# Kernel optimization log

Hardware: AMD Instinct MI355X
Metric: run time of the kernel (lower is better)

The kernel has to match this reference:

```python
import jax, jax.numpy as jnp
import numpy as np

D_MODEL = 1024
N_HEADS = 16
CHUNK = 64
EPS = 1e-6


def elu_plus_1(x):
    return jax.nn.elu(x) + 1.0


def setup_inputs() -> dict:
    key = jax.random.key(0)
    kx, kq, kk, kv, ko = jax.random.split(key, 5)
    B, T = 4, 4096
    # xavier_uniform for square (D, D) weights: limit = sqrt(6/(D+D))
    lim = float(np.sqrt(6.0 / (D_MODEL + D_MODEL)))
    mk = lambda k: jax.random.uniform(k, (D_MODEL, D_MODEL), jnp.float32, -lim, lim)
    return {
        "x": jax.random.normal(kx, (B, T, D_MODEL), jnp.float32),
        "W_q": mk(kq),
        "W_k": mk(kk),
        "W_v": mk(kv),
        "W_o": mk(ko),
    }


def reference(x, W_q, W_k, W_v, W_o):
    B, T, D = x.shape
    H = N_HEADS
    dk = D // H
    dv = dk
    C = CHUNK
    N = T // C  # T chosen divisible by chunk size (no padding needed)

    q = (x @ W_q.T).reshape(B, T, H, dk)
    k = (x @ W_k.T).reshape(B, T, H, dk)
    v = (x @ W_v.T).reshape(B, T, H, dv)

    phi_q = elu_plus_1(q).reshape(B, N, C, H, dk)
    phi_k = elu_plus_1(k).reshape(B, N, C, H, dk)
    vc = v.reshape(B, N, C, H, dv)

    # Per-chunk key-value outer products and key sums, then exclusive prefix
    # sums over chunks give the carried state S and normalizer z at each
    # chunk's start (same math as the sequential chunk loop).
    KV = jnp.einsum('bnchk,bnchv->bnhkv', phi_k, vc)      # (B,N,H,dk,dv)
    Ksum = phi_k.sum(axis=2)                               # (B,N,C->sum,H,dk) -> (B,N,H,dk)
    KV_cum = jnp.cumsum(KV, axis=1)
    Ksum_cum = jnp.cumsum(Ksum, axis=1)
    S_prefix = jnp.concatenate([jnp.zeros_like(KV_cum[:, :1]), KV_cum[:, :-1]], axis=1)
    z_prefix = jnp.concatenate([jnp.zeros_like(Ksum_cum[:, :1]), Ksum_cum[:, :-1]], axis=1)

    # Inter-chunk contribution from carried state
    inter = jnp.einsum('bnchk,bnhkv->bnchv', phi_q, S_prefix)   # (B,N,C,H,dv)
    z_inter = jnp.einsum('bnchk,bnhk->bnch', phi_q, z_prefix)   # (B,N,C,H)

    # Intra-chunk causal attention
    mask = jnp.tril(jnp.ones((C, C), dtype=x.dtype))
    attn = jnp.einsum('bnihk,bnjhk->bnhij', phi_q, phi_k) * mask  # (B,N,H,C,C)
    intra = jnp.einsum('bnhij,bnjhv->bnihv', attn, vc)            # (B,N,C,H,dv)
    z_intra = attn.sum(axis=-1).transpose(0, 1, 3, 2)             # (B,N,C,H)

    denom = jnp.clip((z_inter + z_intra)[..., None], 1e-6, None)
    y = (inter + intra) / denom                                   # (B,N,C,H,dv)
    y = y.reshape(B, T, H * dv)
    return y @ W_o.T
```

## Files before the change

### kernel.cpp

```cpp
#include <hip/hip_runtime.h>


typedef unsigned short u16;
typedef float  f32x4 __attribute__((ext_vector_type(4)));
typedef short  b16x8 __attribute__((ext_vector_type(8)));
typedef u16    u16x4 __attribute__((ext_vector_type(4)));
typedef u16    u16x8 __attribute__((ext_vector_type(8)));

#define DEVINL __device__ __forceinline__

DEVINL u16 f2b(float f) {
  unsigned u = __float_as_uint(f);
  return (u16)((u + 0x7fffu + ((u >> 16) & 1u)) >> 16);
}
DEVINL float b2f(u16 s) { return __uint_as_float(((unsigned)s) << 16); }

DEVINL f32x4 mfma16(b16x8 a, b16x8 b, f32x4 c) {
  return __builtin_amdgcn_mfma_f32_16x16x32_bf16(a, b, c, 0, 0, 0);
}

DEVINL float phi_elu1(float v) { return v > 0.f ? v + 1.f : __expf(v); }

__global__ void cvt_kernel(const float* __restrict__ in, u16* __restrict__ out, int n8) {
  int stride = gridDim.x * blockDim.x;
  for (int i = blockIdx.x * blockDim.x + threadIdx.x; i < n8; i += stride) {
    const float* p = in + (size_t)i * 8;
    f32x4 a = *(const f32x4*)p;
    f32x4 b = *(const f32x4*)(p + 4);
    u16x8 o;
    o[0] = f2b(a[0]); o[1] = f2b(a[1]); o[2] = f2b(a[2]); o[3] = f2b(a[3]);
    o[4] = f2b(b[0]); o[5] = f2b(b[1]); o[6] = f2b(b[2]); o[7] = f2b(b[3]);
    *(u16x8*)(out + (size_t)i * 8) = o;
  }
}

template <bool PHI, typename OT>
__global__ __launch_bounds__(512, 2) void gemm256(const u16* __restrict__ A,
                                                  const u16* __restrict__ B,
                                                  OT* __restrict__ C, int M, int N) {
  __shared__ char lds[131072];
  const int tid = threadIdx.x, wid = tid >> 6, l = tid & 63;
  const int l15 = l & 15, lg = l >> 4;
  const int wr = wid >> 2, wc = wid & 3;
  const int ntn = N >> 8;
  const int nwg = gridDim.x, bid = blockIdx.x;
  const int cpx = nwg >> 3;
  const int sb = (bid & 7) * cpx + (bid >> 3);
  const int tm = sb / ntn, tn = sb - tm * ntn;

  const int colX0 = (lg * 16) ^ ((l15 & 7) << 4);
  const int colX1 = (64 + lg * 16) ^ ((l15 & 7) << 4);
  char* ldsA = lds + wr * 16384 + l15 * 128;
  char* ldsB = lds + 32768 + (wc >> 1) * 16384 + ((wc & 1) * 64 + l15) * 128;

  const int srow = tid >> 3;
  const int scol = ((((tid & 7) * 16) ^ ((srow & 7) << 4)) >> 1);
  const u16* sA = A + (size_t)(tm * 256 + srow) * 1024 + scol;
  const u16* sB = B + (size_t)(tn * 256 + srow) * 1024 + scol;
  char* ldsStage = lds + wid * 1024;

#define STAGE(tt, h)                                                            \
  do {                                                                          \
    const u16* s_ = ((h) < 2 ? sA : sB) + (size_t)(((h) & 1) * 128) * 1024 +    \
                    (size_t)(tt) * 64;                                          \
    char* d_ = ldsStage + (((tt) & 1) << 16) + ((h) < 2 ? 0 : 32768) +          \
               (((h) & 1) << 14);                                               \
    __builtin_amdgcn_global_load_lds(                                           \
        (const __attribute__((address_space(1))) void*)(s_),                    \
        (__attribute__((address_space(3))) void*)(d_), 16, 0, 0);               \
    __builtin_amdgcn_global_load_lds(                                           \
        (const __attribute__((address_space(1))) void*)(s_ + 64 * 1024),        \
        (__attribute__((address_space(3))) void*)(d_ + 8192), 16, 0, 0);        \
  } while (0)

  f32x4 acc[8][4];
#pragma unroll
  for (int i = 0; i < 8; i++)
#pragma unroll
    for (int j = 0; j < 4; j++) acc[i][j] = f32x4{0.f, 0.f, 0.f, 0.f};

  STAGE(0, 0); STAGE(0, 1); STAGE(0, 2); STAGE(0, 3);
  STAGE(1, 2); STAGE(1, 3);
  asm volatile("s_waitcnt vmcnt(4)" ::: "memory");
  __builtin_amdgcn_s_barrier();

  b16x8 a0[4], a1[4], b0[4], b1[4];
  for (int t = 0; t < 16; ++t) {
    const int cb = (t & 1) << 16;
#pragma unroll
    for (int fm = 0; fm < 4; fm++) a0[fm] = *(const b16x8*)(ldsA + cb + fm * 2048 + colX0);
#pragma unroll
    for (int fn = 0; fn < 4; fn++) b0[fn] = *(const b16x8*)(ldsB + cb + fn * 2048 + colX0);
    if (t < 15) STAGE(t + 1, 0);
    __builtin_amdgcn_s_barrier();
    asm volatile("s_waitcnt lgkmcnt(0)" ::: "memory");
    __builtin_amdgcn_sched_barrier(0);
    __builtin_amdgcn_s_setprio(1);
#pragma unroll
    for (int fm = 0; fm < 4; fm++)
#pragma unroll
      for (int fn = 0; fn < 4; fn++) acc[fm][fn] = mfma16(a0[fm], b0[fn], acc[fm][fn]);
    __builtin_amdgcn_s_setprio(0);
    __builtin_amdgcn_s_barrier();
#pragma unroll
    for (int fm = 0; fm < 4; fm++) a1[fm] = *(const b16x8*)(ldsA + cb + (4 + fm) * 2048 + colX0);
#pragma unroll
    for (int fn = 0; fn < 4; fn++) b1[fn] = *(const b16x8*)(ldsB + cb + fn * 2048 + colX1);
    if (t < 15) STAGE(t + 1, 1);
    __builtin_amdgcn_s_barrier();
    asm volatile("s_waitcnt lgkmcnt(0)" ::: "memory");
    __builtin_amdgcn_sched_barrier(0);
    __builtin_amdgcn_s_setprio(1);
#pragma unroll
    for (int fm = 0; fm < 4; fm++)
#pragma unroll
      for (int fn = 0; fn < 4; fn++) acc[4 + fm][fn] = mfma16(a1[fm], b0[fn], acc[4 + fm][fn]);
    __builtin_amdgcn_s_setprio(0);
    __builtin_amdgcn_s_barrier();
#pragma unroll
    for (int fm = 0; fm < 4; fm++) a0[fm] = *(const b16x8*)(ldsA + cb + fm * 2048 + colX1);
    if (t < 14) STAGE(t + 2, 2);
    __builtin_amdgcn_s_barrier();
    asm volatile("s_waitcnt lgkmcnt(0)" ::: "memory");
    __builtin_amdgcn_sched_barrier(0);
    __builtin_amdgcn_s_setprio(1);
#pragma unroll
    for (int fm = 0; fm < 4; fm++)
#pragma unroll
      for (int fn = 0; fn < 4; fn++) acc[fm][fn] = mfma16(a0[fm], b1[fn], acc[fm][fn]);
    __builtin_amdgcn_s_setprio(0);
    __builtin_amdgcn_s_barrier();
#pragma unroll
    for (int fm = 0; fm < 4; fm++) a1[fm] = *(const b16x8*)(ldsA + cb + (4 + fm) * 2048 + colX1);
    if (t < 14) STAGE(t + 2, 3);
    __builtin_amdgcn_s_barrier();
    asm volatile("s_waitcnt lgkmcnt(0)" ::: "memory");
    __builtin_amdgcn_sched_barrier(0);
    __builtin_amdgcn_s_setprio(1);
#pragma unroll
    for (int fm = 0; fm < 4; fm++)
#pragma unroll
      for (int fn = 0; fn < 4; fn++) acc[4 + fm][fn] = mfma16(a1[fm], b1[fn], acc[4 + fm][fn]);
    __builtin_amdgcn_s_setprio(0);
    if (t < 14) asm volatile("s_waitcnt vmcnt(4)" ::: "memory");
    else        asm volatile("s_waitcnt vmcnt(0)" ::: "memory");
    __builtin_amdgcn_s_barrier();
  }
#undef STAGE

#pragma unroll
  for (int fm = 0; fm < 8; ++fm)
#pragma unroll
    for (int fn = 0; fn < 4; ++fn)
#pragma unroll
      for (int r = 0; r < 4; ++r) {
        size_t grow = (size_t)tm * 256 + wr * 128 + fm * 16 + lg * 4 + r;
        size_t gcol = (size_t)tn * 256 + wc * 64 + fn * 16 + l15;
        float v = acc[fm][fn][r];
        if (PHI) v = phi_elu1(v);
        OT* p = C + grow * (size_t)N + gcol;
        if constexpr (sizeof(OT) == 2) *p = (OT)f2b(v);
        else                           *p = (OT)v;
      }
}

__global__ __launch_bounds__(256) void transpose64(const u16* __restrict__ in,
                                                   u16* __restrict__ out) {
  __shared__ u16 tile[64][68];
  const int t = threadIdx.x;
  const int tr = blockIdx.x, tc = blockIdx.y;
#pragma unroll
  for (int i = 0; i < 4; i++) {
    int idx = i * 256 + t, r = idx >> 4, c4 = idx & 15;
    u16x4 v = *(const u16x4*)(in + (size_t)(tr * 64 + r) * 1024 + tc * 64 + c4 * 4);
    *(u16x4*)&tile[r][c4 * 4] = v;
  }
  __syncthreads();
#pragma unroll
  for (int i = 0; i < 4; i++) {
    int idx = i * 256 + t, oc = idx >> 4, r4 = idx & 15;
    u16x4 v;
    v[0] = tile[r4 * 4 + 0][oc]; v[1] = tile[r4 * 4 + 1][oc];
    v[2] = tile[r4 * 4 + 2][oc]; v[3] = tile[r4 * 4 + 3][oc];
    *(u16x4*)(out + (size_t)(tc * 64 + oc) * 16384 + tr * 64 + r4 * 4) = v;
  }
}

__global__ __launch_bounds__(256, 2) void kv_kernel(const u16* __restrict__ kT,
                                                    const u16* __restrict__ vT,
                                                    u16* __restrict__ KVT,
                                                    float* __restrict__ Ksum) {
  const int tid = threadIdx.x, wid = tid >> 6, l = tid & 63, l15 = l & 15, lg = l >> 4;
  const int bid = blockIdx.x, hg = bid & 3, bn = bid >> 2, n = bn & 63, b = bn >> 6;
  const int h = hg * 4 + wid;
  const size_t cb = (size_t)b * 4096 + n * 64 + lg * 8;

  b16x8 af[4][2], bf[4][2];
#pragma unroll
  for (int fm = 0; fm < 4; fm++)
#pragma unroll
    for (int ks = 0; ks < 2; ks++)
      af[fm][ks] = *(const b16x8*)(vT + (size_t)(h * 64 + fm * 16 + l15) * 16384 + cb + ks * 32);
#pragma unroll
  for (int fn = 0; fn < 4; fn++)
#pragma unroll
    for (int ks = 0; ks < 2; ks++)
      bf[fn][ks] = *(const b16x8*)(kT + (size_t)(h * 64 + fn * 16 + l15) * 16384 + cb + ks * 32);

  f32x4 acc[4][4];
#pragma unroll
  for (int i = 0; i < 4; i++)
#pragma unroll
    for (int j = 0; j < 4; j++) acc[i][j] = f32x4{0.f, 0.f, 0.f, 0.f};
#pragma unroll
  for (int ks = 0; ks < 2; ks++)
#pragma unroll
    for (int fm = 0; fm < 4; fm++)
#pragma unroll
      for (int fn = 0; fn < 4; fn++) acc[fm][fn] = mfma16(af[fm][ks], bf[fn][ks], acc[fm][fn]);

  float ksum[4] = {0.f, 0.f, 0.f, 0.f};
#pragma unroll
  for (int fn = 0; fn < 4; fn++) {
#pragma unroll
    for (int ks = 0; ks < 2; ks++)
#pragma unroll
      for (int j = 0; j < 8; j++) ksum[fn] += b2f((u16)bf[fn][ks][j]);
    ksum[fn] += __shfl_xor(ksum[fn], 16);
    ksum[fn] += __shfl_xor(ksum[fn], 32);
  }
  const size_t ob = (size_t)(b * 64 + n) * 16 + h;
  if (l < 16) {
#pragma unroll
    for (int fn = 0; fn < 4; fn++) Ksum[ob * 64 + fn * 16 + l15] = ksum[fn];
  }
#pragma unroll
  for (int fm = 0; fm < 4; fm++)
#pragma unroll
    for (int fn = 0; fn < 4; fn++)
#pragma unroll
      for (int r = 0; r < 4; r++)
        KVT[ob * 4096 + (size_t)(fm * 16 + lg * 4 + r) * 64 + fn * 16 + l15] =
            f2b(acc[fm][fn][r]);
}

__global__ __launch_bounds__(256) void scan_s(const u16* __restrict__ KVT,
                                              u16* __restrict__ ST) {
  const int bh = blockIdx.x >> 4, slice = blockIdx.x & 15;
  const int b = bh >> 4, h = bh & 15;
  const int e = slice * 256 + threadIdx.x;
  float acc = 0.f;
  for (int n = 0; n < 64; n++) {
    size_t idx = ((size_t)(b * 64 + n) * 16 + h) * 4096 + e;
    ST[idx] = f2b(acc);
    acc += b2f(KVT[idx]);
  }
}

__global__ __launch_bounds__(64) void scan_z(const float* __restrict__ Ksum,
                                             float* __restrict__ zpre) {
  const int b = blockIdx.x >> 4, h = blockIdx.x & 15;
  const int t = threadIdx.x;
  float acc = 0.f;
  for (int n = 0; n < 64; n++) {
    size_t idx = ((size_t)(b * 64 + n) * 16 + h) * 64 + t;
    zpre[idx] = acc;
    acc += Ksum[idx];
  }
}

__global__ __launch_bounds__(256, 2) void attn_out(const u16* __restrict__ phiQ,
                                                   const u16* __restrict__ phiK,
                                                   const u16* __restrict__ vT,
                                                   const u16* __restrict__ ST,
                                                   const float* __restrict__ zpre,
                                                   u16* __restrict__ Y) {
  __shared__ char lds[4 * 8192 + 4 * 256];
  const int tid = threadIdx.x, wid = tid >> 6, l = tid & 63, l15 = l & 15, lg = l >> 4;
  const int bid = blockIdx.x, hg = bid & 3, bn = bid >> 2, n = bn & 63, b = bn >> 6;
  const int h = hg * 4 + wid;
  const size_t row0 = (size_t)b * 4096 + n * 64;
  const int dcol = h * 64;

  b16x8 qf[4][2];
#pragma unroll
  for (int fi = 0; fi < 4; fi++)
#pragma unroll
    for (int ks = 0; ks < 2; ks++)
      qf[fi][ks] = *(const b16x8*)(phiQ + (row0 + fi * 16 + l15) * 1024 + dcol + lg * 8 + ks * 32);

  f32x4 accT[4][4];
#pragma unroll
  for (int i = 0; i < 4; i++)
#pragma unroll
    for (int j = 0; j < 4; j++) accT[i][j] = f32x4{0.f, 0.f, 0.f, 0.f};
  {
    b16x8 kf[4][2];
#pragma unroll
    for (int fj = 0; fj < 4; fj++)
#pragma unroll
      for (int ks = 0; ks < 2; ks++)
        kf[fj][ks] = *(const b16x8*)(phiK + (row0 + fj * 16 + l15) * 1024 + dcol + lg * 8 + ks * 32);
#pragma unroll
    for (int ks = 0; ks < 2; ks++)
#pragma unroll
      for (int fj = 0; fj < 4; fj++)
#pragma unroll
        for (int fi = 0; fi < 4; fi++)
          accT[fj][fi] = mfma16(kf[fj][ks], qf[fi][ks], accT[fj][fi]);
  }

  const size_t zb = ((size_t)(b * 64 + n) * 16 + h) * 64;
  float zi[4] = {0.f, 0.f, 0.f, 0.f};
#pragma unroll
  for (int ks = 0; ks < 2; ks++) {
    f32x4 z0 = *(const f32x4*)(zpre + zb + lg * 8 + ks * 32);
    f32x4 z1 = *(const f32x4*)(zpre + zb + lg * 8 + ks * 32 + 4);
#pragma unroll
    for (int fi = 0; fi < 4; fi++)
#pragma unroll
      for (int j = 0; j < 4; j++) {
        zi[fi] += b2f((u16)qf[fi][ks][j])     * z0[j];
        zi[fi] += b2f((u16)qf[fi][ks][j + 4]) * z1[j];
      }
  }

  char* abuf = lds + wid * 8192;
  float zt[4] = {0.f, 0.f, 0.f, 0.f};
#pragma unroll
  for (int fi = 0; fi < 4; fi++) {
    const int i = fi * 16 + l15;
    const int swz = (i & 7) << 4;
#pragma unroll
    for (int fj = 0; fj < 4; fj++) {
      f32x4 v = accT[fj][fi];
#pragma unroll
      for (int r = 0; r < 4; r++) {
        int j = fj * 16 + lg * 4 + r;
        if (j > i) v[r] = 0.f;
        zt[fi] += v[r];
      }
      unsigned w0 = (unsigned)f2b(v[0]) | ((unsigned)f2b(v[1]) << 16);
      unsigned w1 = (unsigned)f2b(v[2]) | ((unsigned)f2b(v[3]) << 16);
      int jb = (fj * 16 + lg * 4) * 2;
      *(unsigned*)(abuf + i * 128 + (jb ^ swz)) = w0;
      *(unsigned*)(abuf + i * 128 + ((jb + 4) ^ swz)) = w1;
    }
  }

  float* dbuf = (float*)(lds + 32768 + wid * 256);
#pragma unroll
  for (int fi = 0; fi < 4; fi++) {
    float z = zi[fi] + zt[fi];
    z += __shfl_xor(z, 16);
    z += __shfl_xor(z, 32);
    float rd = 1.f / fmaxf(z, 1e-6f);
    if (l < 16) dbuf[fi * 16 + l15] = rd;
  }
  __syncthreads();

  b16x8 stf[4][2], vf[4][2];
  const size_t stb = ((size_t)(b * 64 + n) * 16 + h) * 4096;
#pragma unroll
  for (int fn = 0; fn < 4; fn++)
#pragma unroll
    for (int ks = 0; ks < 2; ks++) {
      stf[fn][ks] = *(const b16x8*)(ST + stb + (size_t)(fn * 16 + l15) * 64 + lg * 8 + ks * 32);
      vf[fn][ks]  = *(const b16x8*)(vT + (size_t)(dcol + fn * 16 + l15) * 16384 +
                                    (size_t)b * 4096 + n * 64 + lg * 8 + ks * 32);
    }
  f32x4 acc[4][4];
#pragma unroll
  for (int i = 0; i < 4; i++)
#pragma unroll
    for (int j = 0; j < 4; j++) acc[i][j] = f32x4{0.f, 0.f, 0.f, 0.f};
#pragma unroll
  for (int ks = 0; ks < 2; ks++)
#pragma unroll
    for (int fm = 0; fm < 4; fm++)
#pragma unroll
      for (int fn = 0; fn < 4; fn++) acc[fm][fn] = mfma16(qf[fm][ks], stf[fn][ks], acc[fm][fn]);
#pragma unroll
  for (int fm = 0; fm < 4; fm++) {
    const int i = fm * 16 + l15;
    const int swz = (i & 7) << 4;
#pragma unroll
    for (int ks = 0; ks < 2; ks++) {
      b16x8 af = *(const b16x8*)(abuf + i * 128 + ((ks * 64 + lg * 16) ^ swz));
#pragma unroll
      for (int fn = 0; fn < 4; fn++) acc[fm][fn] = mfma16(af, vf[fn][ks], acc[fm][fn]);
    }
  }

#pragma unroll
  for (int fm = 0; fm < 4; fm++)
#pragma unroll
    for (int r = 0; r < 4; r++) {
      float rd = dbuf[fm * 16 + lg * 4 + r];
#pragma unroll
      for (int fn = 0; fn < 4; fn++)
        Y[(row0 + fm * 16 + lg * 4 + r) * 1024 + dcol + fn * 16 + l15] =
            f2b(acc[fm][fn][r] * rd);
    }
}

extern "C" void kernel_launch(void* const* d_in, const int* in_sizes, int n_in,
                              void* d_out, int out_size, void* d_ws, size_t ws_size,
                              hipStream_t stream) {
  const float* x  = (const float*)d_in[0];
  const float* Wq = (const float*)d_in[1];
  const float* Wk = (const float*)d_in[2];
  const float* Wv = (const float*)d_in[3];
  const float* Wo = (const float*)d_in[4];
  float* out = (float*)d_out;

  char* ws = (char*)d_ws;
  size_t off = 0;
  auto alloc = [&](size_t bytes) -> char* {
    char* p = ws + off;
    off += (bytes + 255) & ~(size_t)255;
    return p;
  };
  u16*   xb   = (u16*)alloc(33554432);
  u16*   wqb  = (u16*)alloc(2097152);
  u16*   wkb  = (u16*)alloc(2097152);
  u16*   wvb  = (u16*)alloc(2097152);
  u16*   wob  = (u16*)alloc(2097152);
  u16*   phiQ = (u16*)alloc(33554432);
  u16*   phiK = (u16*)alloc(33554432);
  u16*   vT   = (u16*)alloc(33554432);
  u16*   kT   = (u16*)alloc(33554432);
  u16*   KVT  = (u16*)alloc(33554432);
  float* Ksum = (float*)alloc(1048576);
  u16*   ST   = (u16*)alloc(33554432);
  float* zpre = (float*)alloc(1048576);
  u16*   y    = xb;

  cvt_kernel<<<2048, 256, 0, stream>>>(x, xb, 2097152);
  cvt_kernel<<<512, 256, 0, stream>>>(Wq, wqb, 131072);
  cvt_kernel<<<512, 256, 0, stream>>>(Wk, wkb, 131072);
  cvt_kernel<<<512, 256, 0, stream>>>(Wv, wvb, 131072);
  cvt_kernel<<<512, 256, 0, stream>>>(Wo, wob, 131072);

  gemm256<true, u16><<<256, 512, 0, stream>>>(xb, wqb, phiQ, 16384, 1024);
  gemm256<true, u16><<<256, 512, 0, stream>>>(xb, wkb, phiK, 16384, 1024);
  gemm256<false, u16><<<256, 512, 0, stream>>>(wvb, xb, vT, 1024, 16384);

  transpose64<<<dim3(256, 16), 256, 0, stream>>>(phiK, kT);
  kv_kernel<<<1024, 256, 0, stream>>>(kT, vT, KVT, Ksum);
  scan_s<<<1024, 256, 0, stream>>>(KVT, ST);
  scan_z<<<64, 64, 0, stream>>>(Ksum, zpre);
  attn_out<<<1024, 256, 0, stream>>>(phiQ, phiK, vT, ST, zpre, y);

  gemm256<false, float><<<256, 512, 0, stream>>>(y, wob, out, 16384, 1024);
}
```

Baseline: 252.3 us.

## Fuse QKV projections into one GEMM, vectorize epilogues, relayout scan buffers

Concatenates Wq/Wk/Wv into one weight buffer and computes all three projections in a single 768-block GEMM launch. Tiles that produce V write it transposed directly. Epilogue stores become 4-wide vector stores by swapping the MFMA operand order, so each lane holds contiguous output columns. The four weight conversions merge into one launch. The KV and Ksum prefix buffers are relaid out so the scans over chunks walk contiguous memory, and scan_s prefetches four chunks ahead. This cuts launch count, makes stores coalesced, and improves scan locality, at the cost of a more complex GEMM with per-tile branching.

```diff
diff --git a/kernel.cpp b/kernel.cpp
--- a/kernel.cpp
+++ b/kernel.cpp
@@ -34,19 +34,44 @@
   }
 }
 
-template <bool PHI, typename OT>
+__global__ void cvt4_kernel(const float* __restrict__ p0, const float* __restrict__ p1,
+                            const float* __restrict__ p2, const float* __restrict__ p3,
+                            u16* __restrict__ o0, u16* __restrict__ o1,
+                            u16* __restrict__ o2, u16* __restrict__ o3) {
+  const float* in; u16* out;
+  switch (blockIdx.y) {
+    case 0: in = p0; out = o0; break;
+    case 1: in = p1; out = o1; break;
+    case 2: in = p2; out = o2; break;
+    default: in = p3; out = o3; break;
+  }
+  int i = blockIdx.x * blockDim.x + threadIdx.x;
+  const float* p = in + (size_t)i * 8;
+  f32x4 a = *(const f32x4*)p;
+  f32x4 b = *(const f32x4*)(p + 4);
+  u16x8 o;
+  o[0] = f2b(a[0]); o[1] = f2b(a[1]); o[2] = f2b(a[2]); o[3] = f2b(a[3]);
+  o[4] = f2b(b[0]); o[5] = f2b(b[1]); o[6] = f2b(b[2]); o[7] = f2b(b[3]);
+  *(u16x8*)(out + (size_t)i * 8) = o;
+}
+
+template <int MODE>
 __global__ __launch_bounds__(512, 2) void gemm256(const u16* __restrict__ A,
                                                   const u16* __restrict__ B,
-                                                  OT* __restrict__ C, int M, int N) {
+                                                  u16* __restrict__ phiQ,
+                                                  u16* __restrict__ phiK,
+                                                  u16* __restrict__ vT,
+                                                  float* __restrict__ Fout) {
   __shared__ char lds[131072];
   const int tid = threadIdx.x, wid = tid >> 6, l = tid & 63;
   const int l15 = l & 15, lg = l >> 4;
   const int wr = wid >> 2, wc = wid & 3;
-  const int ntn = N >> 8;
+  const int ntn = (MODE == 0) ? 12 : 4;
   const int nwg = gridDim.x, bid = blockIdx.x;
   const int cpx = nwg >> 3;
   const int sb = (bid & 7) * cpx + (bid >> 3);
   const int tm = sb / ntn, tn = sb - tm * ntn;
+  const bool isV = (MODE == 0) && (tn >= 8);
 
   const int colX0 = (lg * 16) ^ ((l15 & 7) << 4);
   const int colX1 = (64 + lg * 16) ^ ((l15 & 7) << 4);
@@ -73,6 +98,24 @@
         (__attribute__((address_space(3))) void*)(d_ + 8192), 16, 0, 0);        \
   } while (0)
 
+#define MFMA16Q(AF, BF, ACCBASE)                                                \
+  do {                                                                          \
+    __builtin_amdgcn_s_barrier();                                               \
+    asm volatile("s_waitcnt lgkmcnt(0)" ::: "memory");                          \
+    __builtin_amdgcn_sched_barrier(0);                                          \
+    __builtin_amdgcn_s_setprio(1);                                              \
+    if (!isV) {                                                                 \
+      _Pragma("unroll") for (int fm = 0; fm < 4; fm++)                          \
+        _Pragma("unroll") for (int fn = 0; fn < 4; fn++)                        \
+          acc[ACCBASE + fm][fn] = mfma16(BF[fn], AF[fm], acc[ACCBASE + fm][fn]);\
+    } else {                                                                    \
+      _Pragma("unroll") for (int fm = 0; fm < 4; fm++)                          \
+        _Pragma("unroll") for (int fn = 0; fn < 4; fn++)                        \
+          acc[ACCBASE + fm][fn] = mfma16(AF[fm], BF[fn], acc[ACCBASE + fm][fn]);\
+    }                                                                           \
+    __builtin_amdgcn_s_setprio(0);                                              \
+  } while (0)
+
   f32x4 acc[8][4];
 #pragma unroll
   for (int i = 0; i < 8; i++)
@@ -92,76 +135,68 @@
 #pragma unroll
     for (int fn = 0; fn < 4; fn++) b0[fn] = *(const b16x8*)(ldsB + cb + fn * 2048 + colX0);
     if (t < 15) STAGE(t + 1, 0);
-    __builtin_amdgcn_s_barrier();
-    asm volatile("s_waitcnt lgkmcnt(0)" ::: "memory");
-    __builtin_amdgcn_sched_barrier(0);
-    __builtin_amdgcn_s_setprio(1);
-#pragma unroll
-    for (int fm = 0; fm < 4; fm++)
-#pragma unroll
-      for (int fn = 0; fn < 4; fn++) acc[fm][fn] = mfma16(a0[fm], b0[fn], acc[fm][fn]);
-    __builtin_amdgcn_s_setprio(0);
+    MFMA16Q(a0, b0, 0);
     __builtin_amdgcn_s_barrier();
 #pragma unroll
     for (int fm = 0; fm < 4; fm++) a1[fm] = *(const b16x8*)(ldsA + cb + (4 + fm) * 2048 + colX0);
 #pragma unroll
     for (int fn = 0; fn < 4; fn++) b1[fn] = *(const b16x8*)(ldsB + cb + fn * 2048 + colX1);
     if (t < 15) STAGE(t + 1, 1);
-    __builtin_amdgcn_s_barrier();
-    asm volatile("s_waitcnt lgkmcnt(0)" ::: "memory");
-    __builtin_amdgcn_sched_barrier(0);
-    __builtin_amdgcn_s_setprio(1);
-#pragma unroll
-    for (int fm = 0; fm < 4; fm++)
-#pragma unroll
-      for (int fn = 0; fn < 4; fn++) acc[4 + fm][fn] = mfma16(a1[fm], b0[fn], acc[4 + fm][fn]);
-    __builtin_amdgcn_s_setprio(0);
+    MFMA16Q(a1, b0, 4);
     __builtin_amdgcn_s_barrier();
 #pragma unroll
     for (int fm = 0; fm < 4; fm++) a0[fm] = *(const b16x8*)(ldsA + cb + fm * 2048 + colX1);
     if (t < 14) STAGE(t + 2, 2);
-    __builtin_amdgcn_s_barrier();
-    asm volatile("s_waitcnt lgkmcnt(0)" ::: "memory");
-    __builtin_amdgcn_sched_barrier(0);
-    __builtin_amdgcn_s_setprio(1);
-#pragma unroll
-    for (int fm = 0; fm < 4; fm++)
-#pragma unroll
-      for (int fn = 0; fn < 4; fn++) acc[fm][fn] = mfma16(a0[fm], b1[fn], acc[fm][fn]);
-    __builtin_amdgcn_s_setprio(0);
+    MFMA16Q(a0, b1, 0);
     __builtin_amdgcn_s_barrier();
 #pragma unroll
     for (int fm = 0; fm < 4; fm++) a1[fm] = *(const b16x8*)(ldsA + cb + (4 + fm) * 2048 + colX1);
     if (t < 14) STAGE(t + 2, 3);
-    __builtin_amdgcn_s_barrier();
-    asm volatile("s_waitcnt lgkmcnt(0)" ::: "memory");
-    __builtin_amdgcn_sched_barrier(0);
-    __builtin_amdgcn_s_setprio(1);
-#pragma unroll
-    for (int fm = 0; fm < 4; fm++)
-#pragma unroll
-      for (int fn = 0; fn < 4; fn++) acc[4 + fm][fn] = mfma16(a1[fm], b1[fn], acc[4 + fm][fn]);
-    __builtin_amdgcn_s_setprio(0);
+    MFMA16Q(a1, b1, 4);
     if (t < 14) asm volatile("s_waitcnt vmcnt(4)" ::: "memory");
     else        asm volatile("s_waitcnt vmcnt(0)" ::: "memory");
     __builtin_amdgcn_s_barrier();
   }
 #undef STAGE
-
-#pragma unroll
-  for (int fm = 0; fm < 8; ++fm)
-#pragma unroll
-    for (int fn = 0; fn < 4; ++fn)
-#pragma unroll
-      for (int r = 0; r < 4; ++r) {
-        size_t grow = (size_t)tm * 256 + wr * 128 + fm * 16 + lg * 4 + r;
-        size_t gcol = (size_t)tn * 256 + wc * 64 + fn * 16 + l15;
-        float v = acc[fm][fn][r];
-        if (PHI) v = phi_elu1(v);
-        OT* p = C + grow * (size_t)N + gcol;
-        if constexpr (sizeof(OT) == 2) *p = (OT)f2b(v);
-        else                           *p = (OT)v;
+#undef MFMA16Q
+
+  const int tokenbase = tm * 256 + wr * 128;
+  if constexpr (MODE == 1) {
+#pragma unroll
+    for (int fm = 0; fm < 8; ++fm)
+#pragma unroll
+      for (int fn = 0; fn < 4; ++fn) {
+        size_t token = tokenbase + fm * 16 + l15;
+        size_t wcol = tn * 256 + wc * 64 + fn * 16 + lg * 4;
+        *(f32x4*)(Fout + token * 1024 + wcol) = acc[fm][fn];
       }
+  } else if (!isV) {
+    u16* Cc = (tn < 4) ? phiQ : phiK;
+    const int wbase = (tn & 3) * 256 + wc * 64;
+#pragma unroll
+    for (int fm = 0; fm < 8; ++fm)
+#pragma unroll
+      for (int fn = 0; fn < 4; ++fn) {
+        size_t token = tokenbase + fm * 16 + l15;
+        int wcol = wbase + fn * 16 + lg * 4;
+        u16x4 o;
+#pragma unroll
+        for (int r = 0; r < 4; r++) o[r] = f2b(phi_elu1(acc[fm][fn][r]));
+        *(u16x4*)(Cc + token * 1024 + wcol) = o;
+      }
+  } else {
+#pragma unroll
+    for (int fm = 0; fm < 8; ++fm)
+#pragma unroll
+      for (int fn = 0; fn < 4; ++fn) {
+        size_t tq = tokenbase + fm * 16 + lg * 4;
+        size_t d = (tn - 8) * 256 + wc * 64 + fn * 16 + l15;
+        u16x4 o;
+#pragma unroll
+        for (int r = 0; r < 4; r++) o[r] = f2b(acc[fm][fn][r]);
+        *(u16x4*)(vT + d * 16384 + tq) = o;
+      }
+  }
 }
 
 __global__ __launch_bounds__(256) void transpose64(const u16* __restrict__ in,
@@ -229,7 +264,7 @@
     ksum[fn] += __shfl_xor(ksum[fn], 16);
     ksum[fn] += __shfl_xor(ksum[fn], 32);
   }
-  const size_t ob = (size_t)(b * 64 + n) * 16 + h;
+  const size_t ob = (size_t)(b * 16 + h) * 64 + n;
   if (l < 16) {
 #pragma unroll
     for (int fn = 0; fn < 4; fn++) Ksum[ob * 64 + fn * 16 + l15] = ksum[fn];
@@ -246,24 +281,37 @@
 
 __global__ __launch_bounds__(256) void scan_s(const u16* __restrict__ KVT,
                                               u16* __restrict__ ST) {
-  const int bh = blockIdx.x >> 4, slice = blockIdx.x & 15;
-  const int b = bh >> 4, h = bh & 15;
-  const int e = slice * 256 + threadIdx.x;
+  const size_t base = (size_t)(blockIdx.x >> 4) * 64 * 4096 +
+                      (blockIdx.x & 15) * 256 + threadIdx.x;
   float acc = 0.f;
-  for (int n = 0; n < 64; n++) {
-    size_t idx = ((size_t)(b * 64 + n) * 16 + h) * 4096 + e;
-    ST[idx] = f2b(acc);
-    acc += b2f(KVT[idx]);
+  float v[4], w[4];
+#pragma unroll
+  for (int i = 0; i < 4; i++) v[i] = b2f(KVT[base + (size_t)i * 4096]);
+  for (int n = 0; n < 64; n += 4) {
+    if (n < 60) {
+#pragma unroll
+      for (int i = 0; i < 4; i++) w[i] = b2f(KVT[base + (size_t)(n + 4 + i) * 4096]);
+    } else {
+#pragma unroll
+      for (int i = 0; i < 4; i++) w[i] = 0.f;
+    }
+#pragma unroll
+    for (int i = 0; i < 4; i++) {
+      ST[base + (size_t)(n + i) * 4096] = f2b(acc);
+      acc += v[i];
+    }
+#pragma unroll
+    for (int i = 0; i < 4; i++) v[i] = w[i];
   }
 }
 
 __global__ __launch_bounds__(64) void scan_z(const float* __restrict__ Ksum,
                                              float* __restrict__ zpre) {
-  const int b = blockIdx.x >> 4, h = blockIdx.x & 15;
+  const size_t bh = blockIdx.x;
   const int t = threadIdx.x;
   float acc = 0.f;
   for (int n = 0; n < 64; n++) {
-    size_t idx = ((size_t)(b * 64 + n) * 16 + h) * 64 + t;
+    size_t idx = (bh * 64 + n) * 64 + t;
     zpre[idx] = acc;
     acc += Ksum[idx];
   }
@@ -310,7 +358,7 @@
           accT[fj][fi] = mfma16(kf[fj][ks], qf[fi][ks], accT[fj][fi]);
   }
 
-  const size_t zb = ((size_t)(b * 64 + n) * 16 + h) * 64;
+  const size_t zb = ((size_t)(b * 16 + h) * 64 + n) * 64;
   float zi[4] = {0.f, 0.f, 0.f, 0.f};
 #pragma unroll
   for (int ks = 0; ks < 2; ks++) {
@@ -360,7 +408,7 @@
   __syncthreads();
 
   b16x8 stf[4][2], vf[4][2];
-  const size_t stb = ((size_t)(b * 64 + n) * 16 + h) * 4096;
+  const size_t stb = ((size_t)(b * 16 + h) * 64 + n) * 4096;
 #pragma unroll
   for (int fn = 0; fn < 4; fn++)
 #pragma unroll
@@ -422,9 +470,7 @@
     return p;
   };
   u16*   xb   = (u16*)alloc(33554432);
-  u16*   wqb  = (u16*)alloc(2097152);
-  u16*   wkb  = (u16*)alloc(2097152);
-  u16*   wvb  = (u16*)alloc(2097152);
+  u16*   wcat = (u16*)alloc(6291456);
   u16*   wob  = (u16*)alloc(2097152);
   u16*   phiQ = (u16*)alloc(33554432);
   u16*   phiK = (u16*)alloc(33554432);
@@ -437,14 +483,10 @@
   u16*   y    = xb;
 
   cvt_kernel<<<2048, 256, 0, stream>>>(x, xb, 2097152);
-  cvt_kernel<<<512, 256, 0, stream>>>(Wq, wqb, 131072);
-  cvt_kernel<<<512, 256, 0, stream>>>(Wk, wkb, 131072);
-  cvt_kernel<<<512, 256, 0, stream>>>(Wv, wvb, 131072);
-  cvt_kernel<<<512, 256, 0, stream>>>(Wo, wob, 131072);
-
-  gemm256<true, u16><<<256, 512, 0, stream>>>(xb, wqb, phiQ, 16384, 1024);
-  gemm256<true, u16><<<256, 512, 0, stream>>>(xb, wkb, phiK, 16384, 1024);
-  gemm256<false, u16><<<256, 512, 0, stream>>>(wvb, xb, vT, 1024, 16384);
+  cvt4_kernel<<<dim3(512, 4), 256, 0, stream>>>(
+      Wq, Wk, Wv, Wo, wcat, wcat + 1048576, wcat + 2097152, wob);
+
+  gemm256<0><<<768, 512, 0, stream>>>(xb, wcat, phiQ, phiK, vT, nullptr);
 
   transpose64<<<dim3(256, 16), 256, 0, stream>>>(phiK, kT);
   kv_kernel<<<1024, 256, 0, stream>>>(kT, vT, KVT, Ksum);
@@ -452,5 +494,5 @@
   scan_z<<<64, 64, 0, stream>>>(Ksum, zpre);
   attn_out<<<1024, 256, 0, stream>>>(phiQ, phiK, vT, ST, zpre, y);
 
-  gemm256<false, float><<<256, 512, 0, stream>>>(y, wob, out, 16384, 1024);
-}
+  gemm256<1><<<256, 512, 0, stream>>>(y, wob, nullptr, nullptr, nullptr, out);
+}
```

Measured after the change: 558.0 us. +121.2%, slower.
